# Kernel tuning notes

Measured on AMD Instinct MI355X. Metric: run time of the kernel, lower is better.

The kernel has to match this reference:

```python
import jax, jax.numpy as jnp
import numpy as np

B, T, Dx, H, K = 32, 4096, 128, 128, 10


def setup_inputs() -> dict:
    key = jax.random.key(0)
    ks = jax.random.split(key, 11)
    s = 1.0 / np.sqrt(H)  # PyTorch GRU init range

    def p(k, shape):
        return jax.random.uniform(k, shape, jnp.float32, -s, s)

    return {
        "x": jax.random.normal(ks[0], (B, T, Dx), jnp.float32),
        # forward-direction GRU params (gate order: r, z, n as in PyTorch)
        "W_ih_f": p(ks[1], (3 * H, Dx)),
        "W_hh_f": p(ks[2], (3 * H, H)),
        "b_ih_f": p(ks[3], (3 * H,)),
        "b_hh_f": p(ks[4], (3 * H,)),
        # backward-direction GRU params
        "W_ih_b": p(ks[5], (3 * H, Dx)),
        "W_hh_b": p(ks[6], (3 * H, H)),
        "b_ih_b": p(ks[7], (3 * H,)),
        "b_hh_b": p(ks[8], (3 * H,)),
        # final linear classifier
        "W_fc": p(ks[9], (K, 2 * H)),
        "b_fc": p(ks[10], (K,)),
    }


def _gru_scan(x, Wih, Whh, bih, bhh, reverse):
    """Single-direction GRU over time. x: [B,T,Dx] -> [B,T,H]."""
    # Precompute all input projections at once: [T, B, 3H]
    xp = jnp.einsum('btd,gd->tbg', x, Wih) + bih
    Whh_T = Whh.T
    Hd = Whh.shape[1]

    def cell(h, xt):
        hp = h @ Whh_T + bhh            # [B, 3H]
        xr, xz, xn = jnp.split(xt, 3, axis=-1)
        hr, hz, hn = jnp.split(hp, 3, axis=-1)
        r = jax.nn.sigmoid(xr + hr)
        z = jax.nn.sigmoid(xz + hz)
        n = jnp.tanh(xn + r * hn)
        h_new = (1.0 - z) * n + z * h
        return h_new, h_new

    h0 = jnp.zeros((x.shape[0], Hd), x.dtype)
    _, hs = jax.lax.scan(cell, h0, xp, reverse=reverse)  # [T, B, H]
    return jnp.transpose(hs, (1, 0, 2))


def reference(x, W_ih_f, W_hh_f, b_ih_f, b_hh_f,
              W_ih_b, W_hh_b, b_ih_b, b_hh_b, W_fc, b_fc):
    hf = _gru_scan(x, W_ih_f, W_hh_f, b_ih_f, b_hh_f, reverse=False)
    hb = _gru_scan(x, W_ih_b, W_hh_b, b_ih_b, b_hh_b, reverse=True)
    h = jnp.concatenate([hf, hb], axis=-1)  # [B, T, 2H]
    return h @ W_fc.T + b_fc                # [B, T, K]
```

## Files before the change

### kernel.cpp

```cpp
#include <hip/hip_runtime.h>
#include <cstdint>
#include <cstddef>

#define T_LEN   4096
#define B_SZ    32
#define H_DIM   128
#define DX      128
#define K_CLS   10
#define CHUNK   32
#define NCHUNKS (T_LEN / CHUNK)
#define XA_LD   136
#define XP_LD   520
#define HI_LD   136

typedef _Float16 half2v  __attribute__((ext_vector_type(2)));
typedef _Float16 half4   __attribute__((ext_vector_type(4)));
typedef _Float16 half8   __attribute__((ext_vector_type(8)));
typedef float    floatx4 __attribute__((ext_vector_type(4)));

#define LGKM_BARRIER() do {                                   \
    asm volatile("s_waitcnt lgkmcnt(0)" ::: "memory");        \
    __builtin_amdgcn_s_barrier();                             \
    asm volatile("" ::: "memory");                            \
  } while (0)

__global__ void __launch_bounds__(256) init_out_kernel(float* __restrict__ out,
                                                       const float* __restrict__ bfc) {
  int i = blockIdx.x * 256 + threadIdx.x;
  if (i < B_SZ * T_LEN * K_CLS) out[i] = bfc[i % K_CLS];
}

__global__ void __launch_bounds__(512, 2)
gru_bidir_kernel(const float* __restrict__ x,
                 const float* __restrict__ Wih_f, const float* __restrict__ Whh_f,
                 const float* __restrict__ bih_f, const float* __restrict__ bhh_f,
                 const float* __restrict__ Wih_b, const float* __restrict__ Whh_b,
                 const float* __restrict__ bih_b, const float* __restrict__ bhh_b,
                 const float* __restrict__ Wfc, float* __restrict__ out) {
  const int tid = threadIdx.x;
  const int bid = blockIdx.x;
  const int b   = bid & (B_SZ - 1);
  const int dir = bid >> 5;

  const float* Wih = dir ? Wih_b : Wih_f;
  const float* Whh = dir ? Whh_b : Whh_f;
  const float* bih = dir ? bih_b : bih_f;
  const float* bhh = dir ? bhh_b : bhh_f;

  const int lane = tid & 63;
  const int wv   = tid >> 6;
  const int col  = lane & 15;
  const int quad = lane >> 4;
  const int jloc = wv * 16 + col;

  __shared__ __align__(16) _Float16 xA[CHUNK][XA_LD];
  __shared__ __align__(16) _Float16 xPL[CHUNK][XP_LD];
  __shared__ __align__(16) _Float16 hist[CHUNK + 1][HI_LD];

  const float LOG2E = 1.44269504f;

  half8 whf[3][4];
  half8 wif[3][4];
#pragma unroll
  for (int g = 0; g < 3; ++g) {
    const float gs = (g == 2) ? 2.0f * LOG2E : LOG2E;
#pragma unroll
    for (int kt = 0; kt < 4; ++kt) {
      const float* sh = Whh + (size_t)(g * H_DIM + jloc) * H_DIM + kt * 32 + quad * 8;
      const float* si = Wih + (size_t)(g * H_DIM + jloc) * DX + kt * 32 + quad * 8;
      half8 vh, vi;
#pragma unroll
      for (int e = 0; e < 8; ++e) {
        vh[e] = (_Float16)(sh[e] * gs);
        vi[e] = (_Float16)(si[e] * gs);
      }
      whf[g][kt] = vh;
      wif[g][kt] = vi;
    }
  }
  const float bias_r = (bih[jloc] + bhh[jloc]) * LOG2E;
  const float bias_z = (bih[H_DIM + jloc] + bhh[H_DIM + jloc]) * LOG2E;
  const float bias_n = bih[2 * H_DIM + jloc] * (2.0f * LOG2E);
  const float bhn_s  = bhh[2 * H_DIM + jloc] * (2.0f * LOG2E);
  const floatx4 cNb  = {bhn_s, bhn_s, bhn_s, bhn_s};

  half8 fcf[4];
  if (wv < 2) {
#pragma unroll
    for (int kt = 0; kt < 4; ++kt) {
      half8 v;
#pragma unroll
      for (int e = 0; e < 8; ++e) {
        int k = kt * 32 + quad * 8 + e;
        v[e] = (col < K_CLS) ? (_Float16)Wfc[(size_t)col * (2 * H_DIM) + dir * H_DIM + k]
                             : (_Float16)0.f;
      }
      fcf[kt] = v;
    }
  }

  if (tid < H_DIM) hist[0][tid] = (_Float16)0.f;

  const int s_row = tid >> 4;
  const int cb    = (tid & 15) * 8;
  float4 px0, px1;
  {
    int t0 = dir ? (T_LEN - 1 - s_row) : s_row;
    const float* xr = x + ((size_t)b * T_LEN + t0) * DX + cb;
    px0 = *(const float4*)xr;
    px1 = *(const float4*)(xr + 4);
  }

  float hold = 0.f;
  const floatx4 z4 = {0.f, 0.f, 0.f, 0.f};
  __syncthreads();

  for (int c = 0; c < NCHUNKS; ++c) {
    {
      half8 v;
      v[0] = (_Float16)px0.x; v[1] = (_Float16)px0.y; v[2] = (_Float16)px0.z; v[3] = (_Float16)px0.w;
      v[4] = (_Float16)px1.x; v[5] = (_Float16)px1.y; v[6] = (_Float16)px1.z; v[7] = (_Float16)px1.w;
      *(half8*)&xA[s_row][cb] = v;
    }
    LGKM_BARRIER();

#pragma unroll
    for (int mt = 0; mt < 2; ++mt) {
      half8 af[4];
#pragma unroll
      for (int kt = 0; kt < 4; ++kt)
        af[kt] = *(const half8*)&xA[mt * 16 + col][kt * 32 + quad * 8];
      floatx4 pr = z4, pz = z4, pn = z4;
#pragma unroll
      for (int kt = 0; kt < 4; ++kt) {
        pr = __builtin_amdgcn_mfma_f32_16x16x32_f16(af[kt], wif[0][kt], pr, 0, 0, 0);
        pz = __builtin_amdgcn_mfma_f32_16x16x32_f16(af[kt], wif[1][kt], pz, 0, 0, 0);
        pn = __builtin_amdgcn_mfma_f32_16x16x32_f16(af[kt], wif[2][kt], pn, 0, 0, 0);
      }
#pragma unroll
      for (int i = 0; i < 4; ++i) {
        half4 w;
        w[0] = (_Float16)(pr[i] + bias_r);
        w[1] = (_Float16)(pz[i] + bias_z);
        w[2] = (_Float16)(pn[i] + bias_n);
        w[3] = (_Float16)0.f;
        *(half4*)&xPL[mt * 16 + quad * 4 + i][jloc * 4] = w;
      }
    }

    if (c + 1 < NCHUNKS) {
      int s  = (c + 1) * CHUNK + s_row;
      int t0 = dir ? (T_LEN - 1 - s) : s;
      const float* xr = x + ((size_t)b * T_LEN + t0) * DX + cb;
      px0 = *(const float4*)xr;
      px1 = *(const float4*)(xr + 4);
    }
    LGKM_BARRIER();

    uint2 xv = *(const uint2*)&xPL[0][jloc * 4];

#pragma unroll
    for (int s = 0; s < CHUNK; ++s) {
      half8 haf0 = *(const half8*)&hist[s][quad * 8];
      half8 haf1 = *(const half8*)&hist[s][32 + quad * 8];
      half8 haf2 = *(const half8*)&hist[s][64 + quad * 8];
      half8 haf3 = *(const half8*)&hist[s][96 + quad * 8];
      uint2 xvn = *(const uint2*)&xPL[(s + 1) & (CHUNK - 1)][jloc * 4];

      half2v x01 = __builtin_bit_cast(half2v, xv.x);
      half2v x23 = __builtin_bit_cast(half2v, xv.y);
      float xrf = (float)x01.x;
      float xzf = (float)x01.y;
      float xnf = (float)x23.x;
      floatx4 cR = {xrf, xrf, xrf, xrf};
      floatx4 cZ = {xzf, xzf, xzf, xzf};

      floatx4 cr0 = __builtin_amdgcn_mfma_f32_16x16x32_f16(haf0, whf[0][0], cR, 0, 0, 0);
      floatx4 cr1 = __builtin_amdgcn_mfma_f32_16x16x32_f16(haf1, whf[0][1], z4, 0, 0, 0);
      floatx4 cr2 = __builtin_amdgcn_mfma_f32_16x16x32_f16(haf2, whf[0][2], z4, 0, 0, 0);
      floatx4 cr3 = __builtin_amdgcn_mfma_f32_16x16x32_f16(haf3, whf[0][3], z4, 0, 0, 0);
      floatx4 cz0 = __builtin_amdgcn_mfma_f32_16x16x32_f16(haf0, whf[1][0], cZ, 0, 0, 0);
      floatx4 cz1 = __builtin_amdgcn_mfma_f32_16x16x32_f16(haf1, whf[1][1], z4, 0, 0, 0);
      floatx4 cz2 = __builtin_amdgcn_mfma_f32_16x16x32_f16(haf2, whf[1][2], z4, 0, 0, 0);
      floatx4 cz3 = __builtin_amdgcn_mfma_f32_16x16x32_f16(haf3, whf[1][3], z4, 0, 0, 0);
      floatx4 cn0 = __builtin_amdgcn_mfma_f32_16x16x32_f16(haf0, whf[2][0], cNb, 0, 0, 0);
      floatx4 cn1 = __builtin_amdgcn_mfma_f32_16x16x32_f16(haf1, whf[2][1], z4, 0, 0, 0);
      floatx4 cn2 = __builtin_amdgcn_mfma_f32_16x16x32_f16(haf2, whf[2][2], z4, 0, 0, 0);
      floatx4 cn3 = __builtin_amdgcn_mfma_f32_16x16x32_f16(haf3, whf[2][3], z4, 0, 0, 0);

      float ar  = (cr0[0] + cr1[0]) + (cr2[0] + cr3[0]);
      float rr  = __builtin_amdgcn_rcpf(1.f + __builtin_amdgcn_exp2f(-ar));
      float az  = (cz0[0] + cz1[0]) + (cz2[0] + cz3[0]);
      float zz  = __builtin_amdgcn_rcpf(1.f + __builtin_amdgcn_exp2f(-az));
      float anb = (cn0[0] + cn1[0]) + (cn2[0] + cn3[0]);
      float yn  = fmaf(rr, anb, xnf);
      float t   = __builtin_amdgcn_exp2f(-fmaxf(yn, -80.f));
      float nn  = (1.f - t) * __builtin_amdgcn_rcpf(1.f + t);
      hold = fmaf(zz, hold - nn, nn);

      if (quad == 0) hist[s + 1][jloc] = (_Float16)hold;
      LGKM_BARRIER();
      xv = xvn;
    }

    if (wv < 2) {
      floatx4 fa = z4;
#pragma unroll
      for (int kt = 0; kt < 4; ++kt) {
        half8 af = *(const half8*)&hist[1 + wv * 16 + col][kt * 32 + quad * 8];
        fa = __builtin_amdgcn_mfma_f32_16x16x32_f16(af, fcf[kt], fa, 0, 0, 0);
      }
      if (col < K_CLS) {
#pragma unroll
        for (int i = 0; i < 4; ++i) {
          int t  = c * CHUNK + wv * 16 + quad * 4 + i;
          int tt = dir ? (T_LEN - 1 - t) : t;
          atomicAdd(out + ((size_t)b * T_LEN + tt) * K_CLS + col, fa[i]);
        }
      }
    }
    if (tid >= 256 && tid < 256 + H_DIM) hist[0][tid - 256] = hist[CHUNK][tid - 256];
  }
}

extern "C" void kernel_launch(void* const* d_in, const int* in_sizes, int n_in,
                              void* d_out, int out_size, void* d_ws, size_t ws_size,
                              hipStream_t stream) {
  (void)in_sizes; (void)n_in; (void)d_ws; (void)ws_size; (void)out_size;
  const float* x     = (const float*)d_in[0];
  const float* Wih_f = (const float*)d_in[1];
  const float* Whh_f = (const float*)d_in[2];
  const float* bih_f = (const float*)d_in[3];
  const float* bhh_f = (const float*)d_in[4];
  const float* Wih_b = (const float*)d_in[5];
  const float* Whh_b = (const float*)d_in[6];
  const float* bih_b = (const float*)d_in[7];
  const float* bhh_b = (const float*)d_in[8];
  const float* Wfc   = (const float*)d_in[9];
  const float* bfc   = (const float*)d_in[10];
  float* out = (float*)d_out;

  const int n_out = B_SZ * T_LEN * K_CLS;
  init_out_kernel<<<(n_out + 255) / 256, 256, 0, stream>>>(out, bfc);
  gru_bidir_kernel<<<B_SZ * 2, 512, 0, stream>>>(x, Wih_f, Whh_f, bih_f, bhh_f,
                                                 Wih_b, Whh_b, bih_b, bhh_b, Wfc, out);
}
```

Baseline: 1.728 ms.

## Replace per-step hist LDS reads with one load plus DPP broadcasts; pair xproj rows

In the serial recurrence, each lane now loads only one 16-byte slice of the hidden-state history, and the four MFMA A-operand fragments are assembled with DPP quad-permute broadcasts instead of four separate LDS reads. The input-projection buffer is re-laid out so two timesteps share one 16-byte row, which halves the LDS loads for x projections. The tanh is also rewritten as 2*rcp(1+t)-1 to save an instruction. The aim is to shorten the LDS latency on the critical per-step path, at the cost of sixteen extra DPP moves per step.

```diff
diff --git a/kernel.cpp b/kernel.cpp
--- a/kernel.cpp
+++ b/kernel.cpp
@@ -10,19 +10,22 @@
 #define CHUNK   32
 #define NCHUNKS (T_LEN / CHUNK)
 #define XA_LD   136
-#define XP_LD   520
+#define XPP_LD  1040
 #define HI_LD   136
 
 typedef _Float16 half2v  __attribute__((ext_vector_type(2)));
 typedef _Float16 half4   __attribute__((ext_vector_type(4)));
 typedef _Float16 half8   __attribute__((ext_vector_type(8)));
 typedef float    floatx4 __attribute__((ext_vector_type(4)));
+typedef unsigned int uint4v __attribute__((ext_vector_type(4)));
 
 #define LGKM_BARRIER() do {                                   \
     asm volatile("s_waitcnt lgkmcnt(0)" ::: "memory");        \
     __builtin_amdgcn_s_barrier();                             \
     asm volatile("" ::: "memory");                            \
   } while (0)
+
+#define QB(v, C) ((unsigned)__builtin_amdgcn_update_dpp((int)(v), (int)(v), (C), 0xF, 0xF, false))
 
 __global__ void __launch_bounds__(256) init_out_kernel(float* __restrict__ out,
                                                        const float* __restrict__ bfc) {
@@ -54,7 +57,7 @@
   const int jloc = wv * 16 + col;
 
   __shared__ __align__(16) _Float16 xA[CHUNK][XA_LD];
-  __shared__ __align__(16) _Float16 xPL[CHUNK][XP_LD];
+  __shared__ __align__(16) _Float16 xPP[CHUNK / 2][XPP_LD];
   __shared__ __align__(16) _Float16 hist[CHUNK + 1][HI_LD];
 
   const float LOG2E = 1.44269504f;
@@ -113,6 +116,7 @@
 
   float hold = 0.f;
   const floatx4 z4 = {0.f, 0.f, 0.f, 0.f};
+  const int myoff = (col & 3) * 32 + quad * 8;
   __syncthreads();
 
   for (int c = 0; c < NCHUNKS; ++c) {
@@ -139,12 +143,13 @@
       }
 #pragma unroll
       for (int i = 0; i < 4; ++i) {
+        int row = mt * 16 + quad * 4 + i;
         half4 w;
         w[0] = (_Float16)(pr[i] + bias_r);
         w[1] = (_Float16)(pz[i] + bias_z);
         w[2] = (_Float16)(pn[i] + bias_n);
         w[3] = (_Float16)0.f;
-        *(half4*)&xPL[mt * 16 + quad * 4 + i][jloc * 4] = w;
+        *(half4*)&xPP[row >> 1][jloc * 8 + (row & 1) * 4] = w;
       }
     }
 
@@ -157,21 +162,29 @@
     }
     LGKM_BARRIER();
 
-    uint2 xv = *(const uint2*)&xPL[0][jloc * 4];
+    half8 xq  = *(const half8*)&xPP[0][jloc * 8];
+    half8 xqn = xq;
 
 #pragma unroll
     for (int s = 0; s < CHUNK; ++s) {
-      half8 haf0 = *(const half8*)&hist[s][quad * 8];
-      half8 haf1 = *(const half8*)&hist[s][32 + quad * 8];
-      half8 haf2 = *(const half8*)&hist[s][64 + quad * 8];
-      half8 haf3 = *(const half8*)&hist[s][96 + quad * 8];
-      uint2 xvn = *(const uint2*)&xPL[(s + 1) & (CHUNK - 1)][jloc * 4];
-
-      half2v x01 = __builtin_bit_cast(half2v, xv.x);
-      half2v x23 = __builtin_bit_cast(half2v, xv.y);
-      float xrf = (float)x01.x;
-      float xzf = (float)x01.y;
-      float xnf = (float)x23.x;
+      uint4v ou = __builtin_bit_cast(uint4v, *(const half8*)&hist[s][myoff]);
+      if (((s & 1) == 0) && s < CHUNK - 2)
+        xqn = *(const half8*)&xPP[(s >> 1) + 1][jloc * 8];
+
+      uint4v h0u, h1u, h2u, h3u;
+      h0u.x = QB(ou.x, 0x00); h0u.y = QB(ou.y, 0x00); h0u.z = QB(ou.z, 0x00); h0u.w = QB(ou.w, 0x00);
+      h1u.x = QB(ou.x, 0x55); h1u.y = QB(ou.y, 0x55); h1u.z = QB(ou.z, 0x55); h1u.w = QB(ou.w, 0x55);
+      h2u.x = QB(ou.x, 0xAA); h2u.y = QB(ou.y, 0xAA); h2u.z = QB(ou.z, 0xAA); h2u.w = QB(ou.w, 0xAA);
+      h3u.x = QB(ou.x, 0xFF); h3u.y = QB(ou.y, 0xFF); h3u.z = QB(ou.z, 0xFF); h3u.w = QB(ou.w, 0xFF);
+      half8 haf0 = __builtin_bit_cast(half8, h0u);
+      half8 haf1 = __builtin_bit_cast(half8, h1u);
+      half8 haf2 = __builtin_bit_cast(half8, h2u);
+      half8 haf3 = __builtin_bit_cast(half8, h3u);
+
+      const int sub = (s & 1) * 4;
+      float xrf = (float)xq[sub + 0];
+      float xzf = (float)xq[sub + 1];
+      float xnf = (float)xq[sub + 2];
       floatx4 cR = {xrf, xrf, xrf, xrf};
       floatx4 cZ = {xzf, xzf, xzf, xzf};
 
@@ -195,12 +208,12 @@
       float anb = (cn0[0] + cn1[0]) + (cn2[0] + cn3[0]);
       float yn  = fmaf(rr, anb, xnf);
       float t   = __builtin_amdgcn_exp2f(-fmaxf(yn, -80.f));
-      float nn  = (1.f - t) * __builtin_amdgcn_rcpf(1.f + t);
+      float nn  = fmaf(2.f, __builtin_amdgcn_rcpf(1.f + t), -1.f);
       hold = fmaf(zz, hold - nn, nn);
 
       if (quad == 0) hist[s + 1][jloc] = (_Float16)hold;
       LGKM_BARRIER();
-      xv = xvn;
+      if (s & 1) xq = xqn;
     }
 
     if (wv < 2) {
```

New measurement: 1.981 ms. +14.7%, slower.

## Merge forward and backward GRU directions into one 1024-thread block per batch

Applied to the files above, without the earlier changes.

Launches one 1024-thread block per batch element, with each 512-thread half running one direction, instead of 64 separate 512-thread blocks. Shared buffers are duplicated per half. The per-step barrier now synchronizes both directions, which couples two independent serial recurrences and doubles the threads each barrier waits on. The change also partially unrolls the step loop and simplifies the tanh (drops the clamp and uses 2*rcp-1), which may lose some accuracy or overflow safety for extreme inputs.

```diff
diff --git a/kernel.cpp b/kernel.cpp
--- a/kernel.cpp
+++ b/kernel.cpp
@@ -30,17 +30,18 @@
   if (i < B_SZ * T_LEN * K_CLS) out[i] = bfc[i % K_CLS];
 }
 
-__global__ void __launch_bounds__(512, 2)
+__global__ void __launch_bounds__(1024, 4)
 gru_bidir_kernel(const float* __restrict__ x,
                  const float* __restrict__ Wih_f, const float* __restrict__ Whh_f,
                  const float* __restrict__ bih_f, const float* __restrict__ bhh_f,
                  const float* __restrict__ Wih_b, const float* __restrict__ Whh_b,
                  const float* __restrict__ bih_b, const float* __restrict__ bhh_b,
                  const float* __restrict__ Wfc, float* __restrict__ out) {
-  const int tid = threadIdx.x;
-  const int bid = blockIdx.x;
-  const int b   = bid & (B_SZ - 1);
-  const int dir = bid >> 5;
+  const int tid  = threadIdx.x;
+  const int b    = blockIdx.x;
+  const int grp  = tid >> 9;
+  const int ltid = tid & 511;
+  const int dir  = grp;
 
   const float* Wih = dir ? Wih_b : Wih_f;
   const float* Whh = dir ? Whh_b : Whh_f;
@@ -48,14 +49,14 @@
   const float* bhh = dir ? bhh_b : bhh_f;
 
   const int lane = tid & 63;
-  const int wv   = tid >> 6;
+  const int wv   = ltid >> 6;
   const int col  = lane & 15;
   const int quad = lane >> 4;
   const int jloc = wv * 16 + col;
 
-  __shared__ __align__(16) _Float16 xA[CHUNK][XA_LD];
-  __shared__ __align__(16) _Float16 xPL[CHUNK][XP_LD];
-  __shared__ __align__(16) _Float16 hist[CHUNK + 1][HI_LD];
+  __shared__ __align__(16) _Float16 xA[2][CHUNK][XA_LD];
+  __shared__ __align__(16) _Float16 xPL[2][CHUNK][XP_LD];
+  __shared__ __align__(16) _Float16 hist[2][CHUNK + 1][HI_LD];
 
   const float LOG2E = 1.44269504f;
 
@@ -82,7 +83,6 @@
   const float bias_z = (bih[H_DIM + jloc] + bhh[H_DIM + jloc]) * LOG2E;
   const float bias_n = bih[2 * H_DIM + jloc] * (2.0f * LOG2E);
   const float bhn_s  = bhh[2 * H_DIM + jloc] * (2.0f * LOG2E);
-  const floatx4 cNb  = {bhn_s, bhn_s, bhn_s, bhn_s};
 
   half8 fcf[4];
   if (wv < 2) {
@@ -99,10 +99,10 @@
     }
   }
 
-  if (tid < H_DIM) hist[0][tid] = (_Float16)0.f;
-
-  const int s_row = tid >> 4;
-  const int cb    = (tid & 15) * 8;
+  if (ltid < H_DIM) hist[grp][0][ltid] = (_Float16)0.f;
+
+  const int s_row = ltid >> 4;
+  const int cb    = (ltid & 15) * 8;
   float4 px0, px1;
   {
     int t0 = dir ? (T_LEN - 1 - s_row) : s_row;
@@ -120,7 +120,7 @@
       half8 v;
       v[0] = (_Float16)px0.x; v[1] = (_Float16)px0.y; v[2] = (_Float16)px0.z; v[3] = (_Float16)px0.w;
       v[4] = (_Float16)px1.x; v[5] = (_Float16)px1.y; v[6] = (_Float16)px1.z; v[7] = (_Float16)px1.w;
-      *(half8*)&xA[s_row][cb] = v;
+      *(half8*)&xA[grp][s_row][cb] = v;
     }
     LGKM_BARRIER();
 
@@ -129,7 +129,7 @@
       half8 af[4];
 #pragma unroll
       for (int kt = 0; kt < 4; ++kt)
-        af[kt] = *(const half8*)&xA[mt * 16 + col][kt * 32 + quad * 8];
+        af[kt] = *(const half8*)&xA[grp][mt * 16 + col][kt * 32 + quad * 8];
       floatx4 pr = z4, pz = z4, pn = z4;
 #pragma unroll
       for (int kt = 0; kt < 4; ++kt) {
@@ -144,7 +144,7 @@
         w[1] = (_Float16)(pz[i] + bias_z);
         w[2] = (_Float16)(pn[i] + bias_n);
         w[3] = (_Float16)0.f;
-        *(half4*)&xPL[mt * 16 + quad * 4 + i][jloc * 4] = w;
+        *(half4*)&xPL[grp][mt * 16 + quad * 4 + i][jloc * 4] = w;
       }
     }
 
@@ -157,15 +157,15 @@
     }
     LGKM_BARRIER();
 
-    uint2 xv = *(const uint2*)&xPL[0][jloc * 4];
-
-#pragma unroll
+    uint2 xv = *(const uint2*)&xPL[grp][0][jloc * 4];
+
+#pragma unroll 2
     for (int s = 0; s < CHUNK; ++s) {
-      half8 haf0 = *(const half8*)&hist[s][quad * 8];
-      half8 haf1 = *(const half8*)&hist[s][32 + quad * 8];
-      half8 haf2 = *(const half8*)&hist[s][64 + quad * 8];
-      half8 haf3 = *(const half8*)&hist[s][96 + quad * 8];
-      uint2 xvn = *(const uint2*)&xPL[(s + 1) & (CHUNK - 1)][jloc * 4];
+      half8 haf0 = *(const half8*)&hist[grp][s][quad * 8];
+      half8 haf1 = *(const half8*)&hist[grp][s][32 + quad * 8];
+      half8 haf2 = *(const half8*)&hist[grp][s][64 + quad * 8];
+      half8 haf3 = *(const half8*)&hist[grp][s][96 + quad * 8];
+      uint2 xvn = *(const uint2*)&xPL[grp][(s + 1) & (CHUNK - 1)][jloc * 4];
 
       half2v x01 = __builtin_bit_cast(half2v, xv.x);
       half2v x23 = __builtin_bit_cast(half2v, xv.y);
@@ -174,6 +174,7 @@
       float xnf = (float)x23.x;
       floatx4 cR = {xrf, xrf, xrf, xrf};
       floatx4 cZ = {xzf, xzf, xzf, xzf};
+      floatx4 cN = {bhn_s, bhn_s, bhn_s, bhn_s};
 
       floatx4 cr0 = __builtin_amdgcn_mfma_f32_16x16x32_f16(haf0, whf[0][0], cR, 0, 0, 0);
       floatx4 cr1 = __builtin_amdgcn_mfma_f32_16x16x32_f16(haf1, whf[0][1], z4, 0, 0, 0);
@@ -183,7 +184,7 @@
       floatx4 cz1 = __builtin_amdgcn_mfma_f32_16x16x32_f16(haf1, whf[1][1], z4, 0, 0, 0);
       floatx4 cz2 = __builtin_amdgcn_mfma_f32_16x16x32_f16(haf2, whf[1][2], z4, 0, 0, 0);
       floatx4 cz3 = __builtin_amdgcn_mfma_f32_16x16x32_f16(haf3, whf[1][3], z4, 0, 0, 0);
-      floatx4 cn0 = __builtin_amdgcn_mfma_f32_16x16x32_f16(haf0, whf[2][0], cNb, 0, 0, 0);
+      floatx4 cn0 = __builtin_amdgcn_mfma_f32_16x16x32_f16(haf0, whf[2][0], cN, 0, 0, 0);
       floatx4 cn1 = __builtin_amdgcn_mfma_f32_16x16x32_f16(haf1, whf[2][1], z4, 0, 0, 0);
       floatx4 cn2 = __builtin_amdgcn_mfma_f32_16x16x32_f16(haf2, whf[2][2], z4, 0, 0, 0);
       floatx4 cn3 = __builtin_amdgcn_mfma_f32_16x16x32_f16(haf3, whf[2][3], z4, 0, 0, 0);
@@ -194,11 +195,11 @@
       float zz  = __builtin_amdgcn_rcpf(1.f + __builtin_amdgcn_exp2f(-az));
       float anb = (cn0[0] + cn1[0]) + (cn2[0] + cn3[0]);
       float yn  = fmaf(rr, anb, xnf);
-      float t   = __builtin_amdgcn_exp2f(-fmaxf(yn, -80.f));
-      float nn  = (1.f - t) * __builtin_amdgcn_rcpf(1.f + t);
+      float t   = __builtin_amdgcn_exp2f(-yn);
+      float nn  = fmaf(2.f, __builtin_amdgcn_rcpf(1.f + t), -1.f);
       hold = fmaf(zz, hold - nn, nn);
 
-      if (quad == 0) hist[s + 1][jloc] = (_Float16)hold;
+      if (quad == 0) hist[grp][s + 1][jloc] = (_Float16)hold;
       LGKM_BARRIER();
       xv = xvn;
     }
@@ -207,7 +208,7 @@
       floatx4 fa = z4;
 #pragma unroll
       for (int kt = 0; kt < 4; ++kt) {
-        half8 af = *(const half8*)&hist[1 + wv * 16 + col][kt * 32 + quad * 8];
+        half8 af = *(const half8*)&hist[grp][1 + wv * 16 + col][kt * 32 + quad * 8];
         fa = __builtin_amdgcn_mfma_f32_16x16x32_f16(af, fcf[kt], fa, 0, 0, 0);
       }
       if (col < K_CLS) {
@@ -219,7 +220,7 @@
         }
       }
     }
-    if (tid >= 256 && tid < 256 + H_DIM) hist[0][tid - 256] = hist[CHUNK][tid - 256];
+    if (ltid >= 256 && ltid < 256 + H_DIM) hist[grp][0][ltid - 256] = hist[grp][CHUNK][ltid - 256];
   }
 }
 
@@ -242,6 +243,6 @@
 
   const int n_out = B_SZ * T_LEN * K_CLS;
   init_out_kernel<<<(n_out + 255) / 256, 256, 0, stream>>>(out, bfc);
-  gru_bidir_kernel<<<B_SZ * 2, 512, 0, stream>>>(x, Wih_f, Whh_f, bih_f, bhh_f,
-                                                 Wih_b, Whh_b, bih_b, bhh_b, Wfc, out);
+  gru_bidir_kernel<<<B_SZ, 1024, 0, stream>>>(x, Wih_f, Whh_f, bih_f, bhh_f,
+                                              Wih_b, Whh_b, bih_b, bhh_b, Wfc, out);
 }
```

Measured after the change: 4.155 ms. +140.5%, slower.
